# Performance work log

Hardware: AMD Instinct MI355X
Metric: run time of the kernel (lower is better)

Reference implementation:

```python
import jax, jax.numpy as jnp
import numpy as np
from jax import lax

DN = ('NCHW', 'OIHW', 'NCHW')

def conv(x, w, b, stride):
    y = lax.conv_general_dilated(x, w, window_strides=(stride, stride),
                                 padding='VALID', dimension_numbers=DN)
    return y + b[None, :, None, None]

def setup_inputs() -> dict:
    key = jax.random.key(0)
    ks = jax.random.split(key, 7)
    B = 4096
    def he(k, shape, fan_in):
        return jax.random.normal(k, shape, jnp.float32) * np.sqrt(2.0 / fan_in)
    return {
        'x':  jax.random.normal(ks[0], (B, 3, 48, 64), jnp.float32),
        'w1': he(ks[1], (32, 3, 8, 8), 3 * 8 * 8),
        'b1': jnp.zeros((32,), jnp.float32),
        'w2': he(ks[2], (64, 32, 3, 3), 32 * 3 * 3),
        'b2': jnp.zeros((64,), jnp.float32),
        'w3': he(ks[3], (64, 64, 3, 3), 64 * 3 * 3),
        'b3': jnp.zeros((64,), jnp.float32),
        'w4': he(ks[4], (512, 960), 960),
        'b4': jnp.zeros((512,), jnp.float32),
        'w5': he(ks[5], (2, 512), 512),
        'b5': jnp.zeros((2,), jnp.float32),
    }

def reference(x, w1, b1, w2, b2, w3, b3, w4, b4, w5, b5):
    # conv1 (k8 s4): [B,3,48,64] -> [B,32,11,15]
    x1 = conv(x, w1, b1, 4)
    # side reduction (torch code does this on CPU with python loops):
    # sum over batch and channel dims of pre-ReLU activation, divided by 32
    ave1 = jnp.sum(x1, axis=(0, 1)) / 32.0          # [11,15]
    x2 = jax.nn.relu(x1)
    # conv2 (k3 s2): -> [B,64,5,7]
    x3 = conv(x2, w2, b2, 2)
    ave2 = jnp.sum(x3, axis=(0, 1)) / 64.0          # [5,7]
    x4 = jax.nn.relu(x3)
    # conv3 (k3 s1): -> [B,64,3,5]
    x5 = conv(x4, w3, b3, 1)
    ave3 = jnp.sum(x5, axis=(0, 1)) / 64.0          # [3,5]
    x6 = jax.nn.relu(x5)
    # fc head: flatten (C,H,W order, matching torch) -> 960 -> 512 -> 2
    h = x6.reshape(x6.shape[0], -1)                 # [B,960]
    h = jax.nn.relu(h @ w4.T + b4)
    out = h @ w5.T + b5                             # [B,2]
    return out, ave1, ave2, ave3
```

## Files before the change

### kernel.cpp

```cpp
#include <hip/hip_runtime.h>
#include <hip/hip_bf16.h>

#define BATCH 4096

typedef __attribute__((ext_vector_type(8))) short short8;
typedef __attribute__((ext_vector_type(4))) short short4_t;
typedef __attribute__((ext_vector_type(4))) float f32x4;

#define MFMA_BF16 __builtin_amdgcn_mfma_f32_16x16x32_bf16

#define LBAR() asm volatile("s_waitcnt lgkmcnt(0)\n\ts_barrier" ::: "memory")

__device__ __forceinline__ float frelu(float v) { return v > 0.f ? v : 0.f; }
__device__ __forceinline__ unsigned short f2bf(float f) {
    return __builtin_bit_cast(unsigned short, __float2bfloat16(f));
}

__global__ __launch_bounds__(256) void prep_kernel(const float* __restrict__ w1, const float* __restrict__ w2,
                                                   const float* __restrict__ w3, const float* __restrict__ w4,
                                                   const float* __restrict__ b5,
                                                   unsigned short* __restrict__ w1p, unsigned short* __restrict__ w2p,
                                                   unsigned short* __restrict__ w3p, unsigned short* __restrict__ w4p,
                                                   float* __restrict__ out) {
    int idx = blockIdx.x * 256 + threadIdx.x;
    if (idx < 6144) {
        w1p[idx] = f2bf(w1[idx]);
    } else if (idx < 24576) {
        int j = idx - 6144;
        int oc = j / 288, k = j % 288;
        int khw = k / 32, ic = k % 32;
        w2p[j] = f2bf(w2[oc * 288 + ic * 9 + khw]);
    } else if (idx < 61440) {
        int j = idx - 24576;
        int oc = j / 576, k = j % 576;
        int khw = k / 64, ic = k % 64;
        w3p[j] = f2bf(w3[oc * 576 + ic * 9 + khw]);
    } else if (idx < 552960) {
        int j = idx - 61440;
        int n = j / 960, k = j % 960;
        int pos = k / 64, oc = k % 64;
        w4p[j] = f2bf(w4[n * 960 + oc * 15 + pos]);
    } else if (idx < 561152) {
        int j = idx - 552960;
        out[j] = b5[j & 1];
    } else if (idx < 561367) {
        out[8192 + (idx - 561152)] = 0.f;
    }
}

__global__ __launch_bounds__(256) void fused_convs(const float* __restrict__ x,
                                                   const unsigned short* __restrict__ w1p, const float* __restrict__ b1,
                                                   const unsigned short* __restrict__ w2p, const float* __restrict__ b2,
                                                   const unsigned short* __restrict__ w3p, const float* __restrict__ b3,
                                                   unsigned short* __restrict__ x6, float* __restrict__ redbuf) {
    __shared__ __align__(16) unsigned short S[2][9792];
    const int tid = threadIdx.x;
    const int wave = tid >> 6, lane = tid & 63;
    const int col = lane & 15, quad = lane >> 4;
    const int p = wave & 1;
    const int img = blockIdx.x * 2 + (wave >> 1);

    unsigned short* ub  = S[wave >> 1];
    unsigned short* x2l = ub;
    unsigned short* x4l = ub + 5952;
    float* vrow = redbuf + ((size_t)img * 2 + p) * 216;

    {
        const float4* xs = (const float4*)(x + (size_t)img * 9216);
        #pragma unroll
        for (int b = 0; b < 2; ++b) {
            float4 t[9];
            #pragma unroll
            for (int i = 0; i < 9; ++i) t[i] = xs[(b * 9 + i) * 128 + p * 64 + lane];
            #pragma unroll
            for (int i = 0; i < 9; ++i) {
                const int idx = (b * 9 + i) * 128 + p * 64 + lane;
                const int r = idx >> 4, cf = (idx & 15) * 4;
                short4_t s;
                s[0] = (short)f2bf(t[i].x); s[1] = (short)f2bf(t[i].y);
                s[2] = (short)f2bf(t[i].z); s[3] = (short)f2bf(t[i].w);
                *(short4_t*)(ub + r * 68 + cf) = s;
            }
        }
    }
    LBAR();

    short8 Bf1[2][6];
    #pragma unroll
    for (int nt = 0; nt < 2; ++nt) {
        const unsigned short* wb = w1p + (size_t)(nt * 16 + col) * 192 + quad * 8;
        #pragma unroll
        for (int c = 0; c < 6; ++c) Bf1[nt][c] = *(const short8*)(wb + c * 32);
    }
    f32x4 c1a[6][2] = {};
    #pragma unroll
    for (int ti = 0; ti < 6; ++ti) {
        const int t = ti * 2 + p;
        if (t >= 11) break;
        const int posA = t * 16 + col;
        const int pm = posA < 165 ? posA : 164;
        const int oh = pm / 15, ow = pm % 15;
        #pragma unroll
        for (int c = 0; c < 6; ++c) {
            const int ic = c >> 1;
            const int kh = (c & 1) * 4 + quad;
            const unsigned short* ap = ub + (ic * 48 + oh * 4 + kh) * 68 + ow * 4;
            short8 af;
            *(short4_t*)&af       = *(const short4_t*)ap;
            *((short4_t*)&af + 1) = *(const short4_t*)(ap + 4);
            c1a[ti][0] = MFMA_BF16(af, Bf1[0][c], c1a[ti][0], 0, 0, 0);
            c1a[ti][1] = MFMA_BF16(af, Bf1[1][c], c1a[ti][1], 0, 0, 0);
        }
    }
    LBAR();

    {
        const float bias0 = b1[col], bias1 = b1[col + 16];
        #pragma unroll
        for (int ti = 0; ti < 6; ++ti) {
            const int t = ti * 2 + p;
            if (t >= 11) break;
            #pragma unroll
            for (int r = 0; r < 4; ++r) {
                const int pr = t * 16 + quad * 4 + r;
                float v0 = c1a[ti][0][r] + bias0;
                float v1 = c1a[ti][1][r] + bias1;
                float s = v0 + v1;
                s += __shfl_xor(s, 1); s += __shfl_xor(s, 2);
                s += __shfl_xor(s, 4); s += __shfl_xor(s, 8);
                if (pr < 165) {
                    x2l[pr * 36 + col]      = f2bf(frelu(v0));
                    x2l[pr * 36 + col + 16] = f2bf(frelu(v1));
                    if (col == 0) vrow[pr] = s;
                }
            }
        }
        for (int i = lane; i < 165; i += 64)
            if (((i >> 4) & 1) != p) vrow[i] = 0.f;
    }
    LBAR();

    {
        int aoff[3];
        #pragma unroll
        for (int mt = 0; mt < 3; ++mt) {
            int pp = mt * 16 + col; pp = pp < 35 ? pp : 34;
            aoff[mt] = ((pp / 7) * 30 + (pp % 7) * 2) * 36 + quad * 8;
        }
        f32x4 a2[3][2] = {};
        #pragma unroll
        for (int c = 0; c < 9; ++c) {
            const int koff = ((c / 3) * 15 + (c % 3)) * 36;
            short8 A[3];
            #pragma unroll
            for (int mt = 0; mt < 3; ++mt) {
                const unsigned short* ap = x2l + aoff[mt] + koff;
                *(short4_t*)&A[mt]       = *(const short4_t*)ap;
                *((short4_t*)&A[mt] + 1) = *(const short4_t*)(ap + 4);
            }
            #pragma unroll
            for (int n = 0; n < 2; ++n) {
                short8 Bc = *(const short8*)(w2p + (size_t)(p * 32 + n * 16 + col) * 288 + c * 32 + quad * 8);
                #pragma unroll
                for (int mt = 0; mt < 3; ++mt)
                    a2[mt][n] = MFMA_BF16(A[mt], Bc, a2[mt][n], 0, 0, 0);
            }
        }
        float bv2[2];
        #pragma unroll
        for (int n = 0; n < 2; ++n) bv2[n] = b2[p * 32 + n * 16 + col];
        #pragma unroll
        for (int mt = 0; mt < 3; ++mt) {
            #pragma unroll
            for (int r = 0; r < 4; ++r) {
                const int pr = mt * 16 + quad * 4 + r;
                if (pr < 35) {
                    float s = 0.f;
                    #pragma unroll
                    for (int n = 0; n < 2; ++n) {
                        float v = a2[mt][n][r] + bv2[n];
                        s += v;
                        x4l[pr * 72 + p * 32 + n * 16 + col] = f2bf(frelu(v));
                    }
                    s += __shfl_xor(s, 1); s += __shfl_xor(s, 2);
                    s += __shfl_xor(s, 4); s += __shfl_xor(s, 8);
                    if (col == 0) vrow[165 + pr] = s;
                }
            }
        }
    }
    LBAR();

    {
        int pp = col < 15 ? col : 14;
        const int abase = ((pp / 5) * 7 + (pp % 5)) * 72;
        f32x4 a3[2] = {};
        #pragma unroll
        for (int cc = 0; cc < 9; ++cc) {
            const unsigned short* bp = x4l + abase + ((cc / 3) * 7 + (cc % 3)) * 72 + quad * 8;
            short8 af0 = *(const short8*)bp;
            short8 af1 = *(const short8*)(bp + 32);
            #pragma unroll
            for (int n = 0; n < 2; ++n) {
                const unsigned short* wb = w3p + (size_t)(p * 32 + n * 16 + col) * 576 + quad * 8;
                short8 B0 = *(const short8*)(wb + (2 * cc) * 32);
                short8 B1 = *(const short8*)(wb + (2 * cc + 1) * 32);
                a3[n] = MFMA_BF16(af0, B0, a3[n], 0, 0, 0);
                a3[n] = MFMA_BF16(af1, B1, a3[n], 0, 0, 0);
            }
        }
        float bv3[2];
        #pragma unroll
        for (int n = 0; n < 2; ++n) bv3[n] = b3[p * 32 + n * 16 + col];
        unsigned short* xout = x6 + (size_t)img * 960;
        #pragma unroll
        for (int r = 0; r < 4; ++r) {
            const int pr = quad * 4 + r;
            if (pr < 15) {
                float s = 0.f;
                #pragma unroll
                for (int n = 0; n < 2; ++n) {
                    float v = a3[n][r] + bv3[n];
                    s += v;
                    xout[pr * 64 + p * 32 + n * 16 + col] = f2bf(frelu(v));
                }
                s += __shfl_xor(s, 1); s += __shfl_xor(s, 2);
                s += __shfl_xor(s, 4); s += __shfl_xor(s, 8);
                if (col == 0) vrow[200 + pr] = s;
            }
        }
    }
}

__global__ __launch_bounds__(256) void reduce_aves(const float* __restrict__ redbuf, float* __restrict__ out) {
    const int row = blockIdx.x;
    float s = 0.f;
    for (int i = threadIdx.x; i < 8192; i += 256) s += redbuf[(size_t)i * 216 + row];
    s += __shfl_down(s, 32); s += __shfl_down(s, 16); s += __shfl_down(s, 8);
    s += __shfl_down(s, 4);  s += __shfl_down(s, 2);  s += __shfl_down(s, 1);
    __shared__ float wsum[4];
    if ((threadIdx.x & 63) == 0) wsum[threadIdx.x >> 6] = s;
    __syncthreads();
    if (threadIdx.x == 0)
        out[8192 + row] = (wsum[0] + wsum[1] + wsum[2] + wsum[3]) * (row < 165 ? 0.03125f : 0.015625f);
}

__global__ __launch_bounds__(256) void fc45_mfma(const unsigned short* __restrict__ x6,
                                                 const unsigned short* __restrict__ w4p, const float* __restrict__ b4,
                                                 const float* __restrict__ w5, float* __restrict__ out) {
    __shared__ float outl[32][2];
    const int tid = threadIdx.x;
    const int wave = tid >> 6, lane = tid & 63;
    const int col = lane & 15, quad = lane >> 4;
    if (tid < 64) outl[tid >> 1][tid & 1] = 0.f;
    const int m0 = blockIdx.x * 32;
    const int oc = blockIdx.y * 64 + wave * 16 + col;

    const unsigned short* brow  = w4p + (size_t)oc * 960 + quad * 8;
    const unsigned short* arow0 = x6 + (size_t)(m0 + col) * 960 + quad * 8;
    const unsigned short* arow1 = arow0 + 16 * 960;
    f32x4 acc0 = {}, acc1 = {};
    __syncthreads();
    #pragma unroll 6
    for (int c = 0; c < 30; ++c) {
        short8 Bf = *(const short8*)(brow + c * 32);
        short8 a0 = *(const short8*)(arow0 + c * 32);
        short8 a1 = *(const short8*)(arow1 + c * 32);
        acc0 = MFMA_BF16(a0, Bf, acc0, 0, 0, 0);
        acc1 = MFMA_BF16(a1, Bf, acc1, 0, 0, 0);
    }
    const float bb = b4[oc], u0 = w5[oc], u1 = w5[512 + oc];
    #pragma unroll
    for (int mi = 0; mi < 2; ++mi) {
        const f32x4 acc = mi ? acc1 : acc0;
        #pragma unroll
        for (int r = 0; r < 4; ++r) {
            float h = frelu(acc[r] + bb);
            float l0 = h * u0, l1 = h * u1;
            l0 += __shfl_xor(l0, 1); l0 += __shfl_xor(l0, 2); l0 += __shfl_xor(l0, 4); l0 += __shfl_xor(l0, 8);
            l1 += __shfl_xor(l1, 1); l1 += __shfl_xor(l1, 2); l1 += __shfl_xor(l1, 4); l1 += __shfl_xor(l1, 8);
            if (col == 0) {
                atomicAdd(&outl[mi * 16 + quad * 4 + r][0], l0);
                atomicAdd(&outl[mi * 16 + quad * 4 + r][1], l1);
            }
        }
    }
    __syncthreads();
    if (tid < 64) atomicAdd(&out[(m0 + (tid >> 1)) * 2 + (tid & 1)], outl[tid >> 1][tid & 1]);
}

extern "C" void kernel_launch(void* const* d_in, const int* in_sizes, int n_in,
                              void* d_out, int out_size, void* d_ws, size_t ws_size,
                              hipStream_t stream) {
    const float* x  = (const float*)d_in[0];
    const float* w1 = (const float*)d_in[1];
    const float* b1 = (const float*)d_in[2];
    const float* w2 = (const float*)d_in[3];
    const float* b2 = (const float*)d_in[4];
    const float* w3 = (const float*)d_in[5];
    const float* b3 = (const float*)d_in[6];
    const float* w4 = (const float*)d_in[7];
    const float* b4 = (const float*)d_in[8];
    const float* w5 = (const float*)d_in[9];
    const float* b5 = (const float*)d_in[10];
    float* out = (float*)d_out;

    unsigned short* ws = (unsigned short*)d_ws;
    unsigned short* x6  = ws;
    unsigned short* w1p = ws + 3932160;
    unsigned short* w2p = ws + 3938304;
    unsigned short* w3p = ws + 3956736;
    unsigned short* w4p = ws + 3993600;
    float* redbuf = (float*)((char*)d_ws + 8970240);

    prep_kernel<<<2193, 256, 0, stream>>>(w1, w2, w3, w4, b5, w1p, w2p, w3p, w4p, out);
    fused_convs<<<2048, 256, 0, stream>>>(x, w1p, b1, w2p, b2, w3p, b3, x6, redbuf);
    reduce_aves<<<215, 256, 0, stream>>>(redbuf, out);
    fc45_mfma<<<dim3(128, 8), 256, 0, stream>>>(x6, w4p, b4, w5, out);
}
```

Before: 328.2 us.

## Split fused conv kernel to one image per 128-thread block and prefetch weights

Each block now handles one image with two waves instead of two images with four waves, so barriers only sync the waves that share an image and blocks can be scheduled more finely (launch bounds hint 4 blocks/CU). The input load issues all 18 float4 loads at once rather than in two batches. Conv2 and conv3 weight fragments are loaded into registers up front before the MFMA loops, to hide global-load latency. The trade-off is higher register pressure, which may lower occupancy or cause spills.

Result: no change. 333.4 us (+1.6%).

```diff
diff --git a/kernel.cpp b/kernel.cpp
--- a/kernel.cpp
+++ b/kernel.cpp
@@ -48,73 +48,69 @@
     }
 }
 
-__global__ __launch_bounds__(256) void fused_convs(const float* __restrict__ x,
-                                                   const unsigned short* __restrict__ w1p, const float* __restrict__ b1,
-                                                   const unsigned short* __restrict__ w2p, const float* __restrict__ b2,
-                                                   const unsigned short* __restrict__ w3p, const float* __restrict__ b3,
-                                                   unsigned short* __restrict__ x6, float* __restrict__ redbuf) {
-    __shared__ __align__(16) unsigned short S[2][9792];
+__global__ __launch_bounds__(128, 4) void fused_convs(const float* __restrict__ x,
+                                                      const unsigned short* __restrict__ w1p, const float* __restrict__ b1,
+                                                      const unsigned short* __restrict__ w2p, const float* __restrict__ b2,
+                                                      const unsigned short* __restrict__ w3p, const float* __restrict__ b3,
+                                                      unsigned short* __restrict__ x6, float* __restrict__ redbuf) {
+    __shared__ __align__(16) unsigned short ub[9792];
     const int tid = threadIdx.x;
-    const int wave = tid >> 6, lane = tid & 63;
+    const int lane = tid & 63;
     const int col = lane & 15, quad = lane >> 4;
-    const int p = wave & 1;
-    const int img = blockIdx.x * 2 + (wave >> 1);
-
-    unsigned short* ub  = S[wave >> 1];
+    const int p = tid >> 6;
+    const int img = blockIdx.x;
+
     unsigned short* x2l = ub;
     unsigned short* x4l = ub + 5952;
     float* vrow = redbuf + ((size_t)img * 2 + p) * 216;
 
     {
         const float4* xs = (const float4*)(x + (size_t)img * 9216);
-        #pragma unroll
-        for (int b = 0; b < 2; ++b) {
-            float4 t[9];
-            #pragma unroll
-            for (int i = 0; i < 9; ++i) t[i] = xs[(b * 9 + i) * 128 + p * 64 + lane];
-            #pragma unroll
-            for (int i = 0; i < 9; ++i) {
-                const int idx = (b * 9 + i) * 128 + p * 64 + lane;
-                const int r = idx >> 4, cf = (idx & 15) * 4;
-                short4_t s;
-                s[0] = (short)f2bf(t[i].x); s[1] = (short)f2bf(t[i].y);
-                s[2] = (short)f2bf(t[i].z); s[3] = (short)f2bf(t[i].w);
-                *(short4_t*)(ub + r * 68 + cf) = s;
-            }
+        float4 t[18];
+        #pragma unroll
+        for (int i = 0; i < 18; ++i) t[i] = xs[i * 128 + p * 64 + lane];
+        #pragma unroll
+        for (int i = 0; i < 18; ++i) {
+            const int idx = i * 128 + p * 64 + lane;
+            const int r = idx >> 4, cf = (idx & 15) * 4;
+            short4_t s;
+            s[0] = (short)f2bf(t[i].x); s[1] = (short)f2bf(t[i].y);
+            s[2] = (short)f2bf(t[i].z); s[3] = (short)f2bf(t[i].w);
+            *(short4_t*)(ub + r * 68 + cf) = s;
         }
     }
     LBAR();
 
-    short8 Bf1[2][6];
-    #pragma unroll
-    for (int nt = 0; nt < 2; ++nt) {
-        const unsigned short* wb = w1p + (size_t)(nt * 16 + col) * 192 + quad * 8;
-        #pragma unroll
-        for (int c = 0; c < 6; ++c) Bf1[nt][c] = *(const short8*)(wb + c * 32);
-    }
-    f32x4 c1a[6][2] = {};
-    #pragma unroll
-    for (int ti = 0; ti < 6; ++ti) {
-        const int t = ti * 2 + p;
-        if (t >= 11) break;
-        const int posA = t * 16 + col;
-        const int pm = posA < 165 ? posA : 164;
-        const int oh = pm / 15, ow = pm % 15;
-        #pragma unroll
-        for (int c = 0; c < 6; ++c) {
-            const int ic = c >> 1;
-            const int kh = (c & 1) * 4 + quad;
-            const unsigned short* ap = ub + (ic * 48 + oh * 4 + kh) * 68 + ow * 4;
-            short8 af;
-            *(short4_t*)&af       = *(const short4_t*)ap;
-            *((short4_t*)&af + 1) = *(const short4_t*)(ap + 4);
-            c1a[ti][0] = MFMA_BF16(af, Bf1[0][c], c1a[ti][0], 0, 0, 0);
-            c1a[ti][1] = MFMA_BF16(af, Bf1[1][c], c1a[ti][1], 0, 0, 0);
-        }
-    }
-    LBAR();
-
     {
+        short8 Bf1[2][6];
+        #pragma unroll
+        for (int nt = 0; nt < 2; ++nt) {
+            const unsigned short* wb = w1p + (size_t)(nt * 16 + col) * 192 + quad * 8;
+            #pragma unroll
+            for (int c = 0; c < 6; ++c) Bf1[nt][c] = *(const short8*)(wb + c * 32);
+        }
+        f32x4 c1a[6][2] = {};
+        #pragma unroll
+        for (int ti = 0; ti < 6; ++ti) {
+            const int t = ti * 2 + p;
+            if (t >= 11) break;
+            const int posA = t * 16 + col;
+            const int pm = posA < 165 ? posA : 164;
+            const int oh = pm / 15, ow = pm % 15;
+            #pragma unroll
+            for (int c = 0; c < 6; ++c) {
+                const int ic = c >> 1;
+                const int kh = (c & 1) * 4 + quad;
+                const unsigned short* ap = ub + (ic * 48 + oh * 4 + kh) * 68 + ow * 4;
+                short8 af;
+                *(short4_t*)&af       = *(const short4_t*)ap;
+                *((short4_t*)&af + 1) = *(const short4_t*)(ap + 4);
+                c1a[ti][0] = MFMA_BF16(af, Bf1[0][c], c1a[ti][0], 0, 0, 0);
+                c1a[ti][1] = MFMA_BF16(af, Bf1[1][c], c1a[ti][1], 0, 0, 0);
+            }
+        }
+        LBAR();
+
         const float bias0 = b1[col], bias1 = b1[col + 16];
         #pragma unroll
         for (int ti = 0; ti < 6; ++ti) {
@@ -141,6 +137,12 @@
     LBAR();
 
     {
+        short8 W2[18];
+        #pragma unroll
+        for (int c = 0; c < 9; ++c)
+            #pragma unroll
+            for (int n = 0; n < 2; ++n)
+                W2[c * 2 + n] = *(const short8*)(w2p + (size_t)(p * 32 + n * 16 + col) * 288 + c * 32 + quad * 8);
         int aoff[3];
         #pragma unroll
         for (int mt = 0; mt < 3; ++mt) {
@@ -159,12 +161,10 @@
                 *((short4_t*)&A[mt] + 1) = *(const short4_t*)(ap + 4);
             }
             #pragma unroll
-            for (int n = 0; n < 2; ++n) {
-                short8 Bc = *(const short8*)(w2p + (size_t)(p * 32 + n * 16 + col) * 288 + c * 32 + quad * 8);
+            for (int n = 0; n < 2; ++n)
                 #pragma unroll
                 for (int mt = 0; mt < 3; ++mt)
-                    a2[mt][n] = MFMA_BF16(A[mt], Bc, a2[mt][n], 0, 0, 0);
-            }
+                    a2[mt][n] = MFMA_BF16(A[mt], W2[c * 2 + n], a2[mt][n], 0, 0, 0);
         }
         float bv2[2];
         #pragma unroll
@@ -196,17 +196,18 @@
         const int abase = ((pp / 5) * 7 + (pp % 5)) * 72;
         f32x4 a3[2] = {};
         #pragma unroll
-        for (int cc = 0; cc < 9; ++cc) {
-            const unsigned short* bp = x4l + abase + ((cc / 3) * 7 + (cc % 3)) * 72 + quad * 8;
-            short8 af0 = *(const short8*)bp;
-            short8 af1 = *(const short8*)(bp + 32);
-            #pragma unroll
-            for (int n = 0; n < 2; ++n) {
-                const unsigned short* wb = w3p + (size_t)(p * 32 + n * 16 + col) * 576 + quad * 8;
-                short8 B0 = *(const short8*)(wb + (2 * cc) * 32);
-                short8 B1 = *(const short8*)(wb + (2 * cc + 1) * 32);
-                a3[n] = MFMA_BF16(af0, B0, a3[n], 0, 0, 0);
-                a3[n] = MFMA_BF16(af1, B1, a3[n], 0, 0, 0);
+        for (int n = 0; n < 2; ++n) {
+            short8 W3[18];
+            const unsigned short* wb = w3p + (size_t)(p * 32 + n * 16 + col) * 576 + quad * 8;
+            #pragma unroll
+            for (int k = 0; k < 18; ++k) W3[k] = *(const short8*)(wb + k * 32);
+            #pragma unroll
+            for (int cc = 0; cc < 9; ++cc) {
+                const unsigned short* bp = x4l + abase + ((cc / 3) * 7 + (cc % 3)) * 72 + quad * 8;
+                short8 af0 = *(const short8*)bp;
+                short8 af1 = *(const short8*)(bp + 32);
+                a3[n] = MFMA_BF16(af0, W3[2 * cc],     a3[n], 0, 0, 0);
+                a3[n] = MFMA_BF16(af1, W3[2 * cc + 1], a3[n], 0, 0, 0);
             }
         }
         float bv3[2];
@@ -314,7 +315,7 @@
     float* redbuf = (float*)((char*)d_ws + 8970240);
 
     prep_kernel<<<2193, 256, 0, stream>>>(w1, w2, w3, w4, b5, w1p, w2p, w3p, w4p, out);
-    fused_convs<<<2048, 256, 0, stream>>>(x, w1p, b1, w2p, b2, w3p, b3, x6, redbuf);
+    fused_convs<<<BATCH, 128, 0, stream>>>(x, w1p, b1, w2p, b2, w3p, b3, x6, redbuf);
     reduce_aves<<<215, 256, 0, stream>>>(redbuf, out);
     fc45_mfma<<<dim3(128, 8), 256, 0, stream>>>(x6, w4p, b4, w5, out);
 }
```
